# Optimization experiments

Hardware: AMD Instinct MI355X
Metric: run time of the kernel (lower is better)

Reference implementation:

```python
import jax, jax.numpy as jnp
import numpy as np
import math

B, S, D, H, FF = 2, 2048, 1024, 16, 4096
DH = D // H


def _layernorm(x, g, b, eps=1e-5):
    mu = jnp.mean(x, axis=-1, keepdims=True)
    var = jnp.mean((x - mu) ** 2, axis=-1, keepdims=True)
    return (x - mu) * jax.lax.rsqrt(var + eps) * g + b


def setup_inputs() -> dict:
    key = jax.random.key(0)
    ks = jax.random.split(key, 16)
    sc = 0.02
    inp = {
        "x": jax.random.normal(ks[0], (B, S, D), dtype=jnp.float32),
        "Wq": jax.random.normal(ks[1], (D, D), dtype=jnp.float32) * sc,
        "bq": jnp.zeros((D,), jnp.float32),
        "Wk": jax.random.normal(ks[2], (D, D), dtype=jnp.float32) * sc,
        "bk": jnp.zeros((D,), jnp.float32),
        "Wv": jax.random.normal(ks[3], (D, D), dtype=jnp.float32) * sc,
        "bv": jnp.zeros((D,), jnp.float32),
        "Wo": jax.random.normal(ks[4], (D, D), dtype=jnp.float32) * sc,
        "bo": jnp.zeros((D,), jnp.float32),
        "Er": jax.random.uniform(ks[5], (S, DH), dtype=jnp.float32),  # torch.rand init
        "W1": jax.random.normal(ks[6], (D, FF), dtype=jnp.float32) * sc,
        "b1": jnp.zeros((FF,), jnp.float32),
        "W2": jax.random.normal(ks[7], (FF, D), dtype=jnp.float32) * sc,
        "b2": jnp.zeros((D,), jnp.float32),
        "g1": jnp.ones((D,), jnp.float32),
        "be1": jnp.zeros((D,), jnp.float32),
        "g2": jnp.ones((D,), jnp.float32),
        "be2": jnp.zeros((D,), jnp.float32),
    }
    return inp


def _skew(qer, m):
    # qer: (B,H,S,S); m: (S,S) flipped upper-triangular mask
    qer = qer * m
    qer = jnp.pad(qer, ((0, 0), (0, 0), (0, 0), (1, 0)))  # (B,H,S,S+1)
    qer = qer.reshape(B, H, S + 1, S)
    return qer[:, :, 1:, :]  # (B,H,S,S)


def reference(x, Wq, bq, Wk, bk, Wv, bv, Wo, bo, Er, W1, b1, W2, b2, g1, be1, g2, be2):
    x1 = _layernorm(x, g1, be1)
    q = ((x1 @ Wq + bq) / math.sqrt(DH)).reshape(B, S, H, DH)
    k = (x1 @ Wk + bk).reshape(B, S, H, DH)
    v = (x1 @ Wv + bv).reshape(B, S, H, DH)
    att = jnp.einsum("bshd,bthd->bhst", q, k)  # (B,H,S,S)
    qer = jnp.einsum("bshd,td->bhst", q, Er)   # (B,H,S,S) since S == max_seq_len
    m = jnp.flip(jnp.triu(jnp.ones((S, S), dtype=x.dtype)), axis=0)
    att = att + _skew(qer, m)
    att = jax.nn.softmax(att, axis=-1)
    out = jnp.einsum("bhst,bthd->bshd", att, v).reshape(B, S, D)
    out = out @ Wo + bo
    x2 = x1 + out
    x3 = _layernorm(x2, g2, be2)
    y = x3 + jax.nn.relu(x3 @ W1 + b1) @ W2 + b2
    return y
```

## Files before the change

kernel.cpp:

```cpp
#include <hip/hip_runtime.h>
#include <stdint.h>

typedef unsigned short u16;
typedef __attribute__((ext_vector_type(8))) short short8;
typedef __attribute__((ext_vector_type(8))) __bf16 bf16x8;
typedef __attribute__((ext_vector_type(4))) float floatx4;

#define AS1 __attribute__((address_space(1)))
#define AS3 __attribute__((address_space(3)))

#define QSCALE 0.18033688f

__device__ __forceinline__ u16 f2bf(float f) {
    union { float f; unsigned u; } v; v.f = f;
    return (u16)((v.u + 0x8000u) >> 16);
}

__device__ __forceinline__ void gl_lds16(const void* g, void* lds) {
    __builtin_amdgcn_global_load_lds((const AS1 unsigned int*)(uintptr_t)g,
                                     (AS3 unsigned int*)(uintptr_t)lds, 16, 0, 0);
}

__device__ __forceinline__ floatx4 mfma16(short8 a, short8 b, floatx4 c) {
    return __builtin_amdgcn_mfma_f32_16x16x32_bf16((bf16x8)a, (bf16x8)b, c, 0, 0, 0);
}

__global__ void transpose4_1024(const float* __restrict__ s0, const float* __restrict__ s1,
                                const float* __restrict__ s2, const float* __restrict__ s3,
                                u16* __restrict__ d) {
    __shared__ float tile[32][33];
    const float* srcs[4] = {s0, s1, s2, s3};
    const float* src = srcs[blockIdx.z];
    u16* dst = d + (size_t)blockIdx.z * 1024 * 1024;
    int c0 = blockIdx.x * 32, r0 = blockIdx.y * 32;
    int tx = threadIdx.x, ty = threadIdx.y;
#pragma unroll
    for (int i = 0; i < 4; i++)
        tile[ty + i * 8][tx] = src[(size_t)(r0 + ty + i * 8) * 1024 + c0 + tx];
    __syncthreads();
#pragma unroll
    for (int i = 0; i < 4; i++)
        dst[(size_t)(c0 + ty + i * 8) * 1024 + r0 + tx] = f2bf(tile[tx][ty + i * 8]);
}

__global__ void transpose_f32_to_bf16(const float* __restrict__ src, u16* __restrict__ dst,
                                      int R, int C) {
    __shared__ float tile[32][33];
    int c0 = blockIdx.x * 32, r0 = blockIdx.y * 32;
    int tx = threadIdx.x, ty = threadIdx.y;
#pragma unroll
    for (int i = 0; i < 4; i++)
        tile[ty + i * 8][tx] = src[(size_t)(r0 + ty + i * 8) * C + c0 + tx];
    __syncthreads();
#pragma unroll
    for (int i = 0; i < 4; i++)
        dst[(size_t)(c0 + ty + i * 8) * R + r0 + tx] = f2bf(tile[tx][ty + i * 8]);
}

__global__ void convert_to_bf16(const float* __restrict__ s, u16* __restrict__ d, int n) {
    int i = blockIdx.x * 256 + threadIdx.x;
    if (i < n) d[i] = f2bf(s[i]);
}

__global__ __launch_bounds__(256) void ln_kernel(const float* __restrict__ x,
                                                 const float* __restrict__ g,
                                                 const float* __restrict__ bt,
                                                 float* __restrict__ yf,
                                                 u16* __restrict__ yb) {
    const int row = blockIdx.x, tid = threadIdx.x;
    const float4 xv = ((const float4*)(x + (size_t)row * 1024))[tid];
    float s = xv.x + xv.y + xv.z + xv.w;
    float sq = xv.x * xv.x + xv.y * xv.y + xv.z * xv.z + xv.w * xv.w;
#pragma unroll
    for (int m = 1; m < 64; m <<= 1) { s += __shfl_xor(s, m); sq += __shfl_xor(sq, m); }
    __shared__ float red[8];
    int w = tid >> 6;
    if ((tid & 63) == 0) { red[w] = s; red[4 + w] = sq; }
    __syncthreads();
    s = red[0] + red[1] + red[2] + red[3];
    sq = red[4] + red[5] + red[6] + red[7];
    float mean = s * (1.f / 1024.f);
    float var = sq * (1.f / 1024.f) - mean * mean;
    float rstd = rsqrtf(var + 1e-5f);
    float4 gv = ((const float4*)g)[tid];
    float4 bv = ((const float4*)bt)[tid];
    float4 y;
    y.x = (xv.x - mean) * rstd * gv.x + bv.x;
    y.y = (xv.y - mean) * rstd * gv.y + bv.y;
    y.z = (xv.z - mean) * rstd * gv.z + bv.z;
    y.w = (xv.w - mean) * rstd * gv.w + bv.w;
    ((float4*)(yf + (size_t)row * 1024))[tid] = y;
    ushort4 u;
    u.x = f2bf(y.x); u.y = f2bf(y.y); u.z = f2bf(y.z); u.w = f2bf(y.w);
    ((ushort4*)(yb + (size_t)row * 1024))[tid] = u;
}

__global__ __launch_bounds__(256) void gemm_bt(const u16* __restrict__ A,
                                               const u16* __restrict__ Bt,
                                               const float* __restrict__ bias,
                                               u16* __restrict__ outb,
                                               int M, int N, int K) {
    __shared__ __align__(16) u16 As[128 * 64];
    __shared__ __align__(16) u16 Bs[128 * 64];
    const int tid = threadIdx.x;
    const int w = tid >> 6, l = tid & 63, ln = l & 15, quad = l >> 4;
    const int m0 = blockIdx.y * 128, n0 = blockIdx.x * 128;
    const int wm = (w >> 1) * 64, wn = (w & 1) * 64;
    floatx4 acc[4][4] = {};

    for (int k0 = 0; k0 < K; k0 += 64) {
        __syncthreads();
#pragma unroll
        for (int r = 0; r < 4; r++) {
            int o = tid + r * 256;
            int row = o >> 3, c = (o & 7) ^ (row & 7);
            gl_lds16(&A[(size_t)(m0 + row) * K + k0 + c * 8], &As[(w * 64 + r * 256) * 8]);
            gl_lds16(&Bt[(size_t)(n0 + row) * K + k0 + c * 8], &Bs[(w * 64 + r * 256) * 8]);
        }
        __syncthreads();
#pragma unroll
        for (int kk = 0; kk < 2; kk++) {
            short8 av[4], bv[4];
#pragma unroll
            for (int mt = 0; mt < 4; mt++) {
                int rr = wm + mt * 16 + ln;
                av[mt] = *(const short8*)&As[rr * 64 + (((kk * 4 + quad) ^ (rr & 7)) * 8)];
            }
#pragma unroll
            for (int nt = 0; nt < 4; nt++) {
                int rr = wn + nt * 16 + ln;
                bv[nt] = *(const short8*)&Bs[rr * 64 + (((kk * 4 + quad) ^ (rr & 7)) * 8)];
            }
#pragma unroll
            for (int mt = 0; mt < 4; mt++)
#pragma unroll
                for (int nt = 0; nt < 4; nt++)
                    acc[mt][nt] = mfma16(av[mt], bv[nt], acc[mt][nt]);
        }
    }

#pragma unroll
    for (int nt = 0; nt < 4; nt++) {
        int n = n0 + wn + nt * 16 + ln;
        float bval = bias[n];
#pragma unroll
        for (int mt = 0; mt < 4; mt++) {
#pragma unroll
            for (int r = 0; r < 4; r++) {
                int m = m0 + wm + mt * 16 + quad * 4 + r;
                float v = acc[mt][nt][r] + bval;
                outb[(size_t)m * N + n] = f2bf(fmaxf(v, 0.f));
            }
        }
    }
}

__global__ __launch_bounds__(256) void gemm_qkv(const u16* __restrict__ A,
                                                const u16* __restrict__ Bt,
                                                const float* __restrict__ bq,
                                                const float* __restrict__ bk,
                                                const float* __restrict__ bv,
                                                u16* __restrict__ qb,
                                                u16* __restrict__ kb,
                                                u16* __restrict__ vtb) {
    constexpr int K = 1024;
    __shared__ __align__(16) u16 As[128 * 64];
    __shared__ __align__(16) u16 Bs[128 * 64];
    const int tid = threadIdx.x;
    const int w = tid >> 6, l = tid & 63, ln = l & 15, quad = l >> 4;
    const int m0 = blockIdx.y * 128, n0 = blockIdx.x * 128;
    const int wm = (w >> 1) * 64, wn = (w & 1) * 64;
    floatx4 acc[4][4] = {};

    for (int k0 = 0; k0 < K; k0 += 64) {
        __syncthreads();
#pragma unroll
        for (int r = 0; r < 4; r++) {
            int o = tid + r * 256;
            int row = o >> 3, c = (o & 7) ^ (row & 7);
            gl_lds16(&A[(size_t)(m0 + row) * K + k0 + c * 8], &As[(w * 64 + r * 256) * 8]);
            gl_lds16(&Bt[(size_t)(n0 + row) * K + k0 + c * 8], &Bs[(w * 64 + r * 256) * 8]);
        }
        __syncthreads();
#pragma unroll
        for (int kk = 0; kk < 2; kk++) {
            short8 av[4], bv4[4];
#pragma unroll
            for (int mt = 0; mt < 4; mt++) {
                int rr = wm + mt * 16 + ln;
                av[mt] = *(const short8*)&As[rr * 64 + (((kk * 4 + quad) ^ (rr & 7)) * 8)];
            }
#pragma unroll
            for (int nt = 0; nt < 4; nt++) {
                int rr = wn + nt * 16 + ln;
                bv4[nt] = *(const short8*)&Bs[rr * 64 + (((kk * 4 + quad) ^ (rr & 7)) * 8)];
            }
#pragma unroll
            for (int mt = 0; mt < 4; mt++)
#pragma unroll
                for (int nt = 0; nt < 4; nt++)
                    acc[mt][nt] = mfma16(av[mt], bv4[nt], acc[mt][nt]);
        }
    }

    const int seg = (n0 + wn) >> 10;
#pragma unroll
    for (int nt = 0; nt < 4; nt++) {
        int nl = (n0 + wn + nt * 16 + ln) & 1023;
        float bval = seg == 0 ? bq[nl] : (seg == 1 ? bk[nl] : bv[nl]);
#pragma unroll
        for (int mt = 0; mt < 4; mt++) {
#pragma unroll
            for (int r = 0; r < 4; r++) {
                int m = m0 + wm + mt * 16 + quad * 4 + r;
                float v = acc[mt][nt][r] + bval;
                if (seg == 0) {
                    qb[(size_t)m * 1024 + nl] = f2bf(v * QSCALE);
                } else if (seg == 1) {
                    kb[(size_t)m * 1024 + nl] = f2bf(v);
                } else {
                    int b_ = m >> 11, s = m & 2047, hh = nl >> 6, d = nl & 63;
                    vtb[(((size_t)(b_ * 16 + hh)) * 64 + d) * 2048 + s] = f2bf(v);
                }
            }
        }
    }
}

__global__ __launch_bounds__(256) void gemm_bt64(const u16* __restrict__ A,
                                                 const u16* __restrict__ Bt,
                                                 const float* __restrict__ bias,
                                                 const float* __restrict__ resid,
                                                 float* __restrict__ outf,
                                                 int N, int K) {
    __shared__ __align__(16) u16 As[128 * 64];
    __shared__ __align__(16) u16 Bs[64 * 64];
    const int tid = threadIdx.x;
    const int w = tid >> 6, l = tid & 63, ln = l & 15, quad = l >> 4;
    const int m0 = blockIdx.y * 128, n0 = blockIdx.x * 64;
    const int wm = (w >> 1) * 64, wn = (w & 1) * 32;
    floatx4 acc[4][2] = {};

    for (int k0 = 0; k0 < K; k0 += 64) {
        __syncthreads();
#pragma unroll
        for (int r = 0; r < 4; r++) {
            int o = tid + r * 256;
            int row = o >> 3, c = (o & 7) ^ (row & 7);
            gl_lds16(&A[(size_t)(m0 + row) * K + k0 + c * 8], &As[(w * 64 + r * 256) * 8]);
        }
#pragma unroll
        for (int r = 0; r < 2; r++) {
            int o = tid + r * 256;
            int row = o >> 3, c = (o & 7) ^ (row & 7);
            gl_lds16(&Bt[(size_t)(n0 + row) * K + k0 + c * 8], &Bs[(w * 64 + r * 256) * 8]);
        }
        __syncthreads();
#pragma unroll
        for (int kk = 0; kk < 2; kk++) {
            short8 av[4], bv2[2];
#pragma unroll
            for (int mt = 0; mt < 4; mt++) {
                int rr = wm + mt * 16 + ln;
                av[mt] = *(const short8*)&As[rr * 64 + (((kk * 4 + quad) ^ (rr & 7)) * 8)];
            }
#pragma unroll
            for (int nt = 0; nt < 2; nt++) {
                int rr = wn + nt * 16 + ln;
                bv2[nt] = *(const short8*)&Bs[rr * 64 + (((kk * 4 + quad) ^ (rr & 7)) * 8)];
            }
#pragma unroll
            for (int mt = 0; mt < 4; mt++)
#pragma unroll
                for (int nt = 0; nt < 2; nt++)
                    acc[mt][nt] = mfma16(av[mt], bv2[nt], acc[mt][nt]);
        }
    }

#pragma unroll
    for (int nt = 0; nt < 2; nt++) {
        int n = n0 + wn + nt * 16 + ln;
        float bval = bias[n];
#pragma unroll
        for (int mt = 0; mt < 4; mt++) {
#pragma unroll
            for (int r = 0; r < 4; r++) {
                int m = m0 + wm + mt * 16 + quad * 4 + r;
                outf[(size_t)m * N + n] = acc[mt][nt][r] + bval + resid[(size_t)m * N + n];
            }
        }
    }
}

__global__ __launch_bounds__(512, 4) void attn_kernel(const u16* __restrict__ qb,
                                                      const u16* __restrict__ kb,
                                                      const u16* __restrict__ vtb,
                                                      const u16* __restrict__ erb,
                                                      u16* __restrict__ ob) {
    constexpr int S = 2048, D = 1024;
    const int s0 = blockIdx.x * 128, h = blockIdx.y, b = blockIdx.z;
    const int tid = threadIdx.x, w = tid >> 6, l = tid & 63, ln = l & 15, quad = l >> 4;

    __shared__ __align__(16) u16 Ks[64 * 64];
    __shared__ __align__(16) u16 Vts[64 * 64];
    __shared__ __align__(16) u16 Ps[8][16 * 72];

    const u16* kbase = kb + ((size_t)b * S) * D + h * 64;
    const u16* vtbase = vtb + ((size_t)(b * 16 + h)) * 64 * S;

    const u16* qrow = qb + ((size_t)b * S + s0 + w * 16 + ln) * D + h * 64;
    short8 aq[2];
    aq[0] = *(const short8*)&qrow[quad * 8];
    aq[1] = *(const short8*)&qrow[32 + quad * 8];

    const short8 ones8 = {16256, 16256, 16256, 16256, 16256, 16256, 16256, 16256};

    int srcl[4], carry[4];
#pragma unroll
    for (int r = 0; r < 4; r++) {
        srcl[r] = (l & 48) | ((ln + 15 - quad * 4 - r) & 15);
        carry[r] = (ln - quad * 4 - r) > 0 ? 1 : 0;
    }

    floatx4 accO[4] = {};
    floatx4 accL = {};
    const int srow_base = s0 + w * 16 + quad * 4;

    for (int t0 = 0; t0 < S; t0 += 64) {
        const bool bias_tile = (t0 <= s0 + 64);
        __syncthreads();
        {
            int row = tid >> 3, sc = (tid & 7) ^ (row & 7);
            gl_lds16(&kbase[(size_t)(t0 + row) * D + sc * 8], &Ks[w * 512]);
            gl_lds16(&vtbase[(size_t)row * S + t0 + sc * 8], &Vts[w * 512]);
        }
        __syncthreads();

        floatx4 sacc[4] = {};
#pragma unroll
        for (int kk = 0; kk < 2; kk++)
#pragma unroll
            for (int nt = 0; nt < 4; nt++) {
                int tr = nt * 16 + ln;
                short8 bk = *(const short8*)&Ks[tr * 64 + (((kk * 4 + quad) ^ (tr & 7)) * 8)];
                sacc[nt] = mfma16(aq[kk], bk, sacc[nt]);
            }
        floatx4 gacc[5] = {};
        if (bias_tile) {
            int jw0 = t0 - s0 - w * 16 + 2032;
#pragma unroll
            for (int i = 0; i < 5; i++) {
                int j = jw0 + i * 16 + ln;
                j = j > S - 1 ? S - 1 : j;
                const u16* ep = erb + (size_t)j * 64;
                short8 e0 = *(const short8*)&ep[quad * 8];
                short8 e1 = *(const short8*)&ep[32 + quad * 8];
                gacc[i] = mfma16(aq[0], e0, gacc[i]);
                gacc[i] = mfma16(aq[1], e1, gacc[i]);
            }
        }

#pragma unroll
        for (int r = 0; r < 4; r++) {
            const int rloc = quad * 4 + r;
            const int srow = srow_base + r;
            float sh[5];
            if (bias_tile) {
#pragma unroll
                for (int i = 0; i < 5; i++) sh[i] = __shfl(gacc[i][r], srcl[r]);
            }
#pragma unroll
            for (int nt = 0; nt < 4; nt++) {
                float xv = sacc[nt][r];
                if (bias_tile) {
                    float g = carry[r] ? sh[nt + 1] : sh[nt];
                    bool mk = (t0 + nt * 16 + ln) <= srow;
                    xv += mk ? g : 0.f;
                }
                float p = __builtin_amdgcn_exp2f(xv);
                Ps[w][rloc * 72 + nt * 16 + ln] = f2bf(p);
            }
        }

#pragma unroll
        for (int kk = 0; kk < 2; kk++) {
            short8 pf = *(const short8*)&Ps[w][ln * 72 + kk * 32 + quad * 8];
#pragma unroll
            for (int nt = 0; nt < 4; nt++) {
                int dr = nt * 16 + ln;
                short8 bv = *(const short8*)&Vts[dr * 64 + (((kk * 4 + quad) ^ (dr & 7)) * 8)];
                accO[nt] = mfma16(pf, bv, accO[nt]);
            }
            accL = mfma16(pf, ones8, accL);
        }
    }

#pragma unroll
    for (int r = 0; r < 4; r++) {
        float inv = 1.f / accL[r];
        int srow = srow_base + r;
#pragma unroll
        for (int nt = 0; nt < 4; nt++) {
            ob[((size_t)b * S + srow) * D + h * 64 + nt * 16 + ln] = f2bf(accO[nt][r] * inv);
        }
    }
}

extern "C" void kernel_launch(void* const* d_in, const int* in_sizes, int n_in,
                              void* d_out, int out_size, void* d_ws, size_t ws_size,
                              hipStream_t stream) {
    const float* x   = (const float*)d_in[0];
    const float* Wq  = (const float*)d_in[1];
    const float* bq  = (const float*)d_in[2];
    const float* Wk  = (const float*)d_in[3];
    const float* bk  = (const float*)d_in[4];
    const float* Wv  = (const float*)d_in[5];
    const float* bv  = (const float*)d_in[6];
    const float* Wo  = (const float*)d_in[7];
    const float* bo  = (const float*)d_in[8];
    const float* Er  = (const float*)d_in[9];
    const float* W1  = (const float*)d_in[10];
    const float* b1  = (const float*)d_in[11];
    const float* W2  = (const float*)d_in[12];
    const float* b2  = (const float*)d_in[13];
    const float* g1  = (const float*)d_in[14];
    const float* be1 = (const float*)d_in[15];
    const float* g2  = (const float*)d_in[16];
    const float* be2 = (const float*)d_in[17];
    float* out = (float*)d_out;

    char* ws = (char*)d_ws;
    size_t off = 0;
    auto alloc_f = [&](size_t n) { float* p = (float*)(ws + off); off += n * 4; return p; };
    auto alloc_h = [&](size_t n) { u16* p = (u16*)(ws + off); off += n * 2; return p; };

    float* x1f = alloc_f((size_t)4096 * 1024);
    float* x2f = alloc_f((size_t)4096 * 1024);
    float* x3f = alloc_f((size_t)4096 * 1024);
    u16* x1b = alloc_h((size_t)4096 * 1024);
    u16* x3b = alloc_h((size_t)4096 * 1024);
    u16* qbf = alloc_h((size_t)4096 * 1024);
    u16* kbf = alloc_h((size_t)4096 * 1024);
    u16* vtb = alloc_h((size_t)4096 * 1024);
    u16* aob = alloc_h((size_t)4096 * 1024);
    u16* WqT = alloc_h((size_t)1024 * 1024);
    u16* WkT = alloc_h((size_t)1024 * 1024);
    u16* WvT = alloc_h((size_t)1024 * 1024);
    u16* WoT = alloc_h((size_t)1024 * 1024);
    u16* W1T = alloc_h((size_t)1024 * 4096);
    u16* W2T = alloc_h((size_t)1024 * 4096);
    u16* Erb = alloc_h((size_t)2048 * 64);
    u16* hbf = qbf;
    (void)WkT; (void)WvT;

    dim3 tb(32, 8);
    transpose4_1024<<<dim3(32, 32, 4), tb, 0, stream>>>(Wq, Wk, Wv, Wo, WqT);
    transpose_f32_to_bf16<<<dim3(128, 32), tb, 0, stream>>>(W1, W1T, 1024, 4096);
    transpose_f32_to_bf16<<<dim3(32, 128), tb, 0, stream>>>(W2, W2T, 4096, 1024);
    convert_to_bf16<<<512, 256, 0, stream>>>(Er, Erb, 2048 * 64);

    ln_kernel<<<4096, 256, 0, stream>>>(x, g1, be1, x1f, x1b);

    gemm_qkv<<<dim3(24, 32), 256, 0, stream>>>(x1b, WqT, bq, bk, bv, qbf, kbf, vtb);

    attn_kernel<<<dim3(16, 16, 2), 512, 0, stream>>>(qbf, kbf, vtb, Erb, aob);

    gemm_bt64<<<dim3(16, 32), 256, 0, stream>>>(aob, WoT, bo, x1f, x2f, 1024, 1024);

    ln_kernel<<<4096, 256, 0, stream>>>(x2f, g2, be2, x3f, x3b);

    gemm_bt<<<dim3(32, 32), 256, 0, stream>>>(x3b, W1T, b1, hbf, 4096, 4096, 1024);
    gemm_bt64<<<dim3(16, 32), 256, 0, stream>>>(hbf, W2T, b2, x3f, out, 1024, 4096);
}
```

Baseline: 490.4 us.

## Split attention key range across two blocks and merge partial sums

Each attention block now processes only every other 64-key tile, which doubles the grid from 512 to 1024 blocks. Unnormalized partial outputs and row sums go to fp32 workspace, and a new merge kernel adds the two halves, normalizes them and writes bf16. The aim is more parallelism and better CU occupancy on the 256-CU device. The cost is extra global traffic for the partials and one more kernel launch. The merge without max-rescaling is only valid because the kernel already uses a fixed softmax offset rather than a running max.

```diff
diff --git a/kernel.cpp b/kernel.cpp
--- a/kernel.cpp
+++ b/kernel.cpp
@@ -296,9 +296,11 @@
                                                       const u16* __restrict__ kb,
                                                       const u16* __restrict__ vtb,
                                                       const u16* __restrict__ erb,
-                                                      u16* __restrict__ ob) {
+                                                      float* __restrict__ opart,
+                                                      float* __restrict__ lpart) {
     constexpr int S = 2048, D = 1024;
-    const int s0 = blockIdx.x * 128, h = blockIdx.y, b = blockIdx.z;
+    const int s0 = blockIdx.x * 128, h = blockIdx.y;
+    const int b = blockIdx.z >> 1, half = blockIdx.z & 1;
     const int tid = threadIdx.x, w = tid >> 6, l = tid & 63, ln = l & 15, quad = l >> 4;
 
     __shared__ __align__(16) u16 Ks[64 * 64];
@@ -326,7 +328,8 @@
     floatx4 accL = {};
     const int srow_base = s0 + w * 16 + quad * 4;
 
-    for (int t0 = 0; t0 < S; t0 += 64) {
+    for (int it = 0; it < 16; it++) {
+        const int t0 = (it * 2 + half) * 64;
         const bool bias_tile = (t0 <= s0 + 64);
         __syncthreads();
         {
@@ -395,14 +398,42 @@
         }
     }
 
+    const int grp = ((b * 16 + h) * 16 + blockIdx.x);
+    float* Op = opart + ((size_t)(grp * 2 + half) * 128) * 64;
+    float* Lp = lpart + (size_t)(grp * 2 + half) * 128;
 #pragma unroll
     for (int r = 0; r < 4; r++) {
-        float inv = 1.f / accL[r];
-        int srow = srow_base + r;
-#pragma unroll
-        for (int nt = 0; nt < 4; nt++) {
-            ob[((size_t)b * S + srow) * D + h * 64 + nt * 16 + ln] = f2bf(accO[nt][r] * inv);
-        }
+        int rloc = w * 16 + quad * 4 + r;
+#pragma unroll
+        for (int nt = 0; nt < 4; nt++)
+            Op[(size_t)rloc * 64 + nt * 16 + ln] = accO[nt][r];
+        if (ln == 0) Lp[rloc] = accL[r];
+    }
+}
+
+__global__ __launch_bounds__(256) void attn_merge(const float* __restrict__ opart,
+                                                  const float* __restrict__ lpart,
+                                                  u16* __restrict__ ob) {
+    const int grp = blockIdx.x;
+    const int stile = grp & 15, h = (grp >> 4) & 15, b = grp >> 8;
+    const float4* O0 = (const float4*)(opart + ((size_t)(grp * 2 + 0) * 128) * 64);
+    const float4* O1 = (const float4*)(opart + ((size_t)(grp * 2 + 1) * 128) * 64);
+    const float* L0 = lpart + (size_t)(grp * 2 + 0) * 128;
+    const float* L1 = lpart + (size_t)(grp * 2 + 1) * 128;
+    const int tid = threadIdx.x;
+#pragma unroll
+    for (int i = 0; i < 8; i++) {
+        int idx = tid + i * 256;
+        int row = idx >> 4, c4 = idx & 15;
+        float4 o0 = O0[idx], o1 = O1[idx];
+        float inv = 1.f / (L0[row] + L1[row]);
+        ushort4 u;
+        u.x = f2bf((o0.x + o1.x) * inv);
+        u.y = f2bf((o0.y + o1.y) * inv);
+        u.z = f2bf((o0.z + o1.z) * inv);
+        u.w = f2bf((o0.w + o1.w) * inv);
+        int srow = stile * 128 + row;
+        *(ushort4*)&ob[((size_t)b * 2048 + srow) * 1024 + h * 64 + c4 * 4] = u;
     }
 }
 
@@ -450,6 +481,8 @@
     u16* W1T = alloc_h((size_t)1024 * 4096);
     u16* W2T = alloc_h((size_t)1024 * 4096);
     u16* Erb = alloc_h((size_t)2048 * 64);
+    float* opart = alloc_f((size_t)1024 * 128 * 64);
+    float* lpart = alloc_f((size_t)1024 * 128);
     u16* hbf = qbf;
     (void)WkT; (void)WvT;
 
@@ -463,7 +496,8 @@
 
     gemm_qkv<<<dim3(24, 32), 256, 0, stream>>>(x1b, WqT, bq, bk, bv, qbf, kbf, vtb);
 
-    attn_kernel<<<dim3(16, 16, 2), 512, 0, stream>>>(qbf, kbf, vtb, Erb, aob);
+    attn_kernel<<<dim3(16, 16, 4), 512, 0, stream>>>(qbf, kbf, vtb, Erb, opart, lpart);
+    attn_merge<<<512, 256, 0, stream>>>(opart, lpart, aob);
 
     gemm_bt64<<<dim3(16, 32), 256, 0, stream>>>(aob, WoT, bo, x1f, x2f, 1024, 1024);
 
```

Measured after the change: 498.8 us. No clear change (+1.7%).

## Load attention K/V fragments directly from global memory, dropping LDS staging

Applied to the files above, without the earlier changes.

The attention kernel no longer stages K and V^T tiles in shared memory. Each wave now loads its MFMA B-operand fragments straight from global memory into registers, which removes both block-wide barriers per key tile. Blocks shrink to 64 query rows with 4 waves, and the grid doubles to keep total work the same. The trade-off is that each wave re-reads the same K/V tile from global/L2 with no reuse across waves, and register pressure rises.

```diff
diff --git a/kernel.cpp b/kernel.cpp
--- a/kernel.cpp
+++ b/kernel.cpp
@@ -292,18 +292,16 @@
     }
 }
 
-__global__ __launch_bounds__(512, 4) void attn_kernel(const u16* __restrict__ qb,
-                                                      const u16* __restrict__ kb,
-                                                      const u16* __restrict__ vtb,
-                                                      const u16* __restrict__ erb,
-                                                      u16* __restrict__ ob) {
+__global__ __launch_bounds__(256) void attn_kernel(const u16* __restrict__ qb,
+                                                   const u16* __restrict__ kb,
+                                                   const u16* __restrict__ vtb,
+                                                   const u16* __restrict__ erb,
+                                                   u16* __restrict__ ob) {
     constexpr int S = 2048, D = 1024;
-    const int s0 = blockIdx.x * 128, h = blockIdx.y, b = blockIdx.z;
+    const int s0 = blockIdx.x * 64, h = blockIdx.y, b = blockIdx.z;
     const int tid = threadIdx.x, w = tid >> 6, l = tid & 63, ln = l & 15, quad = l >> 4;
 
-    __shared__ __align__(16) u16 Ks[64 * 64];
-    __shared__ __align__(16) u16 Vts[64 * 64];
-    __shared__ __align__(16) u16 Ps[8][16 * 72];
+    __shared__ __align__(16) u16 Ps[4][16 * 72];
 
     const u16* kbase = kb + ((size_t)b * S) * D + h * 64;
     const u16* vtbase = vtb + ((size_t)(b * 16 + h)) * 64 * S;
@@ -326,25 +324,31 @@
     floatx4 accL = {};
     const int srow_base = s0 + w * 16 + quad * 4;
 
+#pragma unroll 1
     for (int t0 = 0; t0 < S; t0 += 64) {
-        const bool bias_tile = (t0 <= s0 + 64);
-        __syncthreads();
-        {
-            int row = tid >> 3, sc = (tid & 7) ^ (row & 7);
-            gl_lds16(&kbase[(size_t)(t0 + row) * D + sc * 8], &Ks[w * 512]);
-            gl_lds16(&vtbase[(size_t)row * S + t0 + sc * 8], &Vts[w * 512]);
-        }
-        __syncthreads();
+        const bool bias_tile = (t0 <= s0);
+
+        short8 kf[2][4], vf[2][4];
+#pragma unroll
+        for (int nt = 0; nt < 4; nt++) {
+            const u16* kr = kbase + (size_t)(t0 + nt * 16 + ln) * D;
+            kf[0][nt] = *(const short8*)&kr[quad * 8];
+            kf[1][nt] = *(const short8*)&kr[32 + quad * 8];
+        }
+#pragma unroll
+        for (int nt = 0; nt < 4; nt++) {
+            const u16* vr = vtbase + (size_t)(nt * 16 + ln) * S + t0;
+            vf[0][nt] = *(const short8*)&vr[quad * 8];
+            vf[1][nt] = *(const short8*)&vr[32 + quad * 8];
+        }
 
         floatx4 sacc[4] = {};
 #pragma unroll
         for (int kk = 0; kk < 2; kk++)
 #pragma unroll
-            for (int nt = 0; nt < 4; nt++) {
-                int tr = nt * 16 + ln;
-                short8 bk = *(const short8*)&Ks[tr * 64 + (((kk * 4 + quad) ^ (tr & 7)) * 8)];
-                sacc[nt] = mfma16(aq[kk], bk, sacc[nt]);
-            }
+            for (int nt = 0; nt < 4; nt++)
+                sacc[nt] = mfma16(aq[kk], kf[kk][nt], sacc[nt]);
+
         floatx4 gacc[5] = {};
         if (bias_tile) {
             int jw0 = t0 - s0 - w * 16 + 2032;
@@ -386,11 +390,8 @@
         for (int kk = 0; kk < 2; kk++) {
             short8 pf = *(const short8*)&Ps[w][ln * 72 + kk * 32 + quad * 8];
 #pragma unroll
-            for (int nt = 0; nt < 4; nt++) {
-                int dr = nt * 16 + ln;
-                short8 bv = *(const short8*)&Vts[dr * 64 + (((kk * 4 + quad) ^ (dr & 7)) * 8)];
-                accO[nt] = mfma16(pf, bv, accO[nt]);
-            }
+            for (int nt = 0; nt < 4; nt++)
+                accO[nt] = mfma16(pf, vf[kk][nt], accO[nt]);
             accL = mfma16(pf, ones8, accL);
         }
     }
@@ -463,7 +464,7 @@
 
     gemm_qkv<<<dim3(24, 32), 256, 0, stream>>>(x1b, WqT, bq, bk, bv, qbf, kbf, vtb);
 
-    attn_kernel<<<dim3(16, 16, 2), 512, 0, stream>>>(qbf, kbf, vtb, Erb, aob);
+    attn_kernel<<<dim3(32, 16, 2), 256, 0, stream>>>(qbf, kbf, vtb, Erb, aob);
 
     gemm_bt64<<<dim3(16, 32), 256, 0, stream>>>(aob, WoT, bo, x1f, x2f, 1024, 1024);
 
```

After: 774.4 us. 1.58x slower.
